# Performance work log

Measured on AMD Instinct MI355X. Metric: run time of the kernel, lower is better.

Reference implementation:

```python
import jax, jax.numpy as jnp
import numpy as np

NTOKENS = 102400
NHID = 128
NTOK_PER_CLASS = 320
NCLASSES = int(np.ceil(NTOKENS / NTOK_PER_CLASS))  # 320
NTOKENS_ACTUAL = NCLASSES * NTOK_PER_CLASS          # 102400
BATCH = 1024


def setup_inputs() -> dict:
    key = jax.random.key(0)
    k1, k2, k3 = jax.random.split(key, 3)
    initrange = 0.1
    return {
        "inputs": jax.random.normal(k1, (BATCH, NHID), dtype=jnp.float32),
        "layer_top_W": jax.random.uniform(k2, (NHID, NCLASSES), dtype=jnp.float32, minval=-initrange, maxval=initrange),
        "layer_top_b": jnp.zeros((NCLASSES,), dtype=jnp.float32),
        "layer_bottom_W": jax.random.uniform(k3, (NTOK_PER_CLASS, NHID), dtype=jnp.float32, minval=-initrange, maxval=initrange),
        "layer_bottom_b": jnp.zeros((NCLASSES,), dtype=jnp.float32),
    }


def reference(inputs, layer_top_W, layer_top_b, layer_bottom_W, layer_bottom_b):
    # labels = arange(ntokens_actual); pos_top = labels // per_class; pos_bottom = labels % per_class
    # The original gathers layer_bottom_W[pos_bottom] ([ntokens_actual, nhid]) before a full matmul;
    # mathematically this is the small matmul inputs @ bottom_W.T tiled nclasses times along dim 1.
    batch = inputs.shape[0]
    pos_bottom_base = jnp.arange(NTOK_PER_CLASS)  # bottom-index pattern within one class block

    layer_top_logits = inputs @ layer_top_W + layer_top_b            # [B, nclasses]
    bottom_block = inputs @ layer_bottom_W.T + layer_bottom_b[pos_bottom_base]  # [B, per_class]

    # repeat_interleave(top, per_class, dim=1) + tile(bottom, nclasses) fused via broadcast:
    target_logits = (layer_top_logits[:, :, None] + bottom_block[:, None, :]).reshape(
        batch, NTOKENS_ACTUAL
    )  # [B, ntokens_actual]
    return target_logits
```

## Files before the change

### kernel.cpp

```cpp
#include <hip/hip_runtime.h>


#define BATCH       1024
#define NHID        128
#define NCLASSES    320
#define PER_CLASS   320
#define ROW_ELEMS   (NCLASSES * PER_CLASS)
#define ROW_F4      (ROW_ELEMS / 4)
#define HALVES      2
#define CLS_PER_BLK (NCLASSES / HALVES)
#define THREADS     320
#define PC_F4       (PER_CLASS / 4)
#define C_PER_ITER  (THREADS / PC_F4)
#define NITER       (CLS_PER_BLK / C_PER_ITER)

typedef float f32x4 __attribute__((ext_vector_type(4)));

__global__ __launch_bounds__(THREADS) void hs_fused_kernel(
    const float* __restrict__ inputs,
    const float* __restrict__ top_W,
    const float* __restrict__ top_b,
    const float* __restrict__ bottom_W,
    const float* __restrict__ bottom_b,
    float* __restrict__ out)
{
    __shared__ __align__(16) float s_in[NHID];
    __shared__ float s_top[CLS_PER_BLK];
    __shared__ __align__(16) float s_bot[PER_CLASS];

    const int b   = blockIdx.x;
    const int h   = blockIdx.y;
    const int tid = threadIdx.x;

    if (tid < NHID) s_in[tid] = inputs[b * NHID + tid];
    __syncthreads();

    for (int j = tid; j < CLS_PER_BLK + PER_CLASS; j += THREADS) {
        float acc;
        if (j < CLS_PER_BLK) {
            const int c = h * CLS_PER_BLK + j;
            acc = top_b[c];
            #pragma unroll 8
            for (int k = 0; k < NHID; ++k)
                acc += s_in[k] * top_W[k * NCLASSES + c];
            s_top[j] = acc;
        } else {
            const int t = j - CLS_PER_BLK;
            acc = bottom_b[t];
            const f32x4* w4 = (const f32x4*)(bottom_W + t * NHID);
            #pragma unroll 8
            for (int k4 = 0; k4 < NHID / 4; ++k4) {
                f32x4 w = w4[k4];
                acc += s_in[4 * k4 + 0] * w.x + s_in[4 * k4 + 1] * w.y
                     + s_in[4 * k4 + 2] * w.z + s_in[4 * k4 + 3] * w.w;
            }
            s_bot[t] = acc;
        }
    }
    __syncthreads();

    const int c_off = tid / PC_F4;
    const int t4    = tid - c_off * PC_F4;
    const f32x4 bv  = ((const f32x4*)s_bot)[t4];

    f32x4* outp = (f32x4*)out
                + (size_t)b * ROW_F4
                + h * (CLS_PER_BLK * PC_F4)
                + c_off * PC_F4 + t4;

    #pragma unroll 8
    for (int it = 0; it < NITER; ++it) {
        const float tv = s_top[it * C_PER_ITER + c_off];
        f32x4 v;
        v.x = tv + bv.x;
        v.y = tv + bv.y;
        v.z = tv + bv.z;
        v.w = tv + bv.w;
        outp[it * (C_PER_ITER * PC_F4)] = v;
    }
}

extern "C" void kernel_launch(void* const* d_in, const int* in_sizes, int n_in,
                              void* d_out, int out_size, void* d_ws, size_t ws_size,
                              hipStream_t stream) {
    const float* inputs   = (const float*)d_in[0];
    const float* top_W    = (const float*)d_in[1];
    const float* top_b    = (const float*)d_in[2];
    const float* bottom_W = (const float*)d_in[3];
    const float* bottom_b = (const float*)d_in[4];
    float* out = (float*)d_out;

    hs_fused_kernel<<<dim3(BATCH, HALVES), THREADS, 0, stream>>>(
        inputs, top_W, top_b, bottom_W, bottom_b, out);
}
```

Baseline: 441.7 us.

## Split into logits kernel plus grid-stride broadcast store kernel via workspace

Splits the work in two. A first kernel computes the top and bottom logits for each batch row into a workspace buffer. A second kernel, run on a fixed grid of 2048 blocks, grid-strides over the output and writes the broadcast sums, so the 400 MB output write is decoupled from the per-row matvec. The old fused kernel is kept as a fallback for when no workspace is available. The cost is an extra launch, integer divisions per element in the store kernel, and small reads of the workspace.

New measurement: 458.2 us. 3.7% more time.

```diff
diff --git a/kernel.cpp b/kernel.cpp
--- a/kernel.cpp
+++ b/kernel.cpp
@@ -1,48 +1,109 @@
 #include <hip/hip_runtime.h>
 
 
-#define BATCH       1024
-#define NHID        128
-#define NCLASSES    320
-#define PER_CLASS   320
-#define ROW_ELEMS   (NCLASSES * PER_CLASS)
-#define ROW_F4      (ROW_ELEMS / 4)
-#define HALVES      2
-#define CLS_PER_BLK (NCLASSES / HALVES)
-#define THREADS     320
-#define PC_F4       (PER_CLASS / 4)
-#define C_PER_ITER  (THREADS / PC_F4)
-#define NITER       (CLS_PER_BLK / C_PER_ITER)
+#define BATCH      1024
+#define NHID       128
+#define NCLASSES   320
+#define PER_CLASS  320
+#define ROW_ELEMS  (NCLASSES * PER_CLASS)
+#define ROW_F4     (ROW_ELEMS / 4)
+#define PC_F4      (PER_CLASS / 4)
+#define LPR        (NCLASSES + PER_CLASS)
+#define LPR_F4     (LPR / 4)
+#define WS_BYTES   ((size_t)BATCH * LPR * sizeof(float))
+
+#define STHREADS   256
+#define SGRID      2048
+#define TOTAL_F4   (BATCH * ROW_F4)
+#define SSTRIDE    (SGRID * STHREADS)
+#define SITERS     (TOTAL_F4 / SSTRIDE)
 
 typedef float f32x4 __attribute__((ext_vector_type(4)));
 
-__global__ __launch_bounds__(THREADS) void hs_fused_kernel(
+__global__ __launch_bounds__(LPR) void hs_logits_kernel(
     const float* __restrict__ inputs,
     const float* __restrict__ top_W,
     const float* __restrict__ top_b,
     const float* __restrict__ bottom_W,
     const float* __restrict__ bottom_b,
-    float* __restrict__ out)
+    float* __restrict__ ws)
 {
     __shared__ __align__(16) float s_in[NHID];
-    __shared__ float s_top[CLS_PER_BLK];
-    __shared__ __align__(16) float s_bot[PER_CLASS];
-
     const int b   = blockIdx.x;
-    const int h   = blockIdx.y;
     const int tid = threadIdx.x;
 
     if (tid < NHID) s_in[tid] = inputs[b * NHID + tid];
     __syncthreads();
 
-    for (int j = tid; j < CLS_PER_BLK + PER_CLASS; j += THREADS) {
+    float acc;
+    if (tid < NCLASSES) {
+        acc = top_b[tid];
+        #pragma unroll 8
+        for (int k = 0; k < NHID; ++k)
+            acc += s_in[k] * top_W[k * NCLASSES + tid];
+    } else {
+        const int t = tid - NCLASSES;
+        acc = bottom_b[t];
+        const f32x4* w4 = (const f32x4*)(bottom_W + t * NHID);
+        #pragma unroll 8
+        for (int k4 = 0; k4 < NHID / 4; ++k4) {
+            f32x4 w = w4[k4];
+            acc += s_in[4*k4+0]*w.x + s_in[4*k4+1]*w.y
+                 + s_in[4*k4+2]*w.z + s_in[4*k4+3]*w.w;
+        }
+    }
+    ws[b * LPR + tid] = acc;
+}
+
+__global__ __launch_bounds__(STHREADS, 8) void hs_stream_kernel(
+    const float* __restrict__ ws,
+    float* __restrict__ out)
+{
+    const f32x4* __restrict__ ws4  = (const f32x4*)ws;
+    f32x4* __restrict__ out4 = (f32x4*)out;
+
+    unsigned g = blockIdx.x * STHREADS + threadIdx.x;
+    #pragma unroll 5
+    for (int it = 0; it < SITERS; ++it, g += SSTRIDE) {
+        const unsigned b  = g / ROW_F4;
+        const unsigned r  = g - b * ROW_F4;
+        const unsigned c  = r / PC_F4;
+        const unsigned t4 = r - c * PC_F4;
+        const float tv = ws[b * LPR + c];
+        const f32x4 bv = ws4[b * LPR_F4 + (NCLASSES/4) + t4];
+        f32x4 v;
+        v.x = tv + bv.x;
+        v.y = tv + bv.y;
+        v.z = tv + bv.z;
+        v.w = tv + bv.w;
+        out4[g] = v;
+    }
+}
+
+#define HALVES      2
+#define CLS_PER_BLK (NCLASSES / HALVES)
+#define FTHREADS    320
+#define C_PER_ITER  (FTHREADS / PC_F4)
+#define NITER       (CLS_PER_BLK / C_PER_ITER)
+
+__global__ __launch_bounds__(FTHREADS) void hs_fused_kernel(
+    const float* __restrict__ inputs, const float* __restrict__ top_W,
+    const float* __restrict__ top_b, const float* __restrict__ bottom_W,
+    const float* __restrict__ bottom_b, float* __restrict__ out)
+{
+    __shared__ __align__(16) float s_in[NHID];
+    __shared__ float s_top[CLS_PER_BLK];
+    __shared__ __align__(16) float s_bot[PER_CLASS];
+    const int b = blockIdx.x, h = blockIdx.y, tid = threadIdx.x;
+    if (tid < NHID) s_in[tid] = inputs[b * NHID + tid];
+    __syncthreads();
+    for (int j = tid; j < CLS_PER_BLK + PER_CLASS; j += FTHREADS) {
         float acc;
         if (j < CLS_PER_BLK) {
             const int c = h * CLS_PER_BLK + j;
             acc = top_b[c];
             #pragma unroll 8
-            for (int k = 0; k < NHID; ++k)
-                acc += s_in[k] * top_W[k * NCLASSES + c];
+            for (int k = 0; k < NHID; ++k) acc += s_in[k] * top_W[k * NCLASSES + c];
             s_top[j] = acc;
         } else {
             const int t = j - CLS_PER_BLK;
@@ -51,31 +112,21 @@
             #pragma unroll 8
             for (int k4 = 0; k4 < NHID / 4; ++k4) {
                 f32x4 w = w4[k4];
-                acc += s_in[4 * k4 + 0] * w.x + s_in[4 * k4 + 1] * w.y
-                     + s_in[4 * k4 + 2] * w.z + s_in[4 * k4 + 3] * w.w;
+                acc += s_in[4*k4+0]*w.x + s_in[4*k4+1]*w.y + s_in[4*k4+2]*w.z + s_in[4*k4+3]*w.w;
             }
             s_bot[t] = acc;
         }
     }
     __syncthreads();
-
     const int c_off = tid / PC_F4;
     const int t4    = tid - c_off * PC_F4;
     const f32x4 bv  = ((const f32x4*)s_bot)[t4];
-
-    f32x4* outp = (f32x4*)out
-                + (size_t)b * ROW_F4
-                + h * (CLS_PER_BLK * PC_F4)
-                + c_off * PC_F4 + t4;
-
+    f32x4* outp = (f32x4*)out + (size_t)b * ROW_F4 + h * (CLS_PER_BLK * PC_F4) + c_off * PC_F4 + t4;
     #pragma unroll 8
     for (int it = 0; it < NITER; ++it) {
         const float tv = s_top[it * C_PER_ITER + c_off];
         f32x4 v;
-        v.x = tv + bv.x;
-        v.y = tv + bv.y;
-        v.z = tv + bv.z;
-        v.w = tv + bv.w;
+        v.x = tv + bv.x; v.y = tv + bv.y; v.z = tv + bv.z; v.w = tv + bv.w;
         outp[it * (C_PER_ITER * PC_F4)] = v;
     }
 }
@@ -90,6 +141,12 @@
     const float* bottom_b = (const float*)d_in[4];
     float* out = (float*)d_out;
 
-    hs_fused_kernel<<<dim3(BATCH, HALVES), THREADS, 0, stream>>>(
-        inputs, top_W, top_b, bottom_W, bottom_b, out);
+    if (d_ws != nullptr && ws_size >= WS_BYTES) {
+        float* ws = (float*)d_ws;
+        hs_logits_kernel<<<BATCH, LPR, 0, stream>>>(inputs, top_W, top_b, bottom_W, bottom_b, ws);
+        hs_stream_kernel<<<SGRID, STHREADS, 0, stream>>>(ws, out);
+    } else {
+        hs_fused_kernel<<<dim3(BATCH, HALVES), FTHREADS, 0, stream>>>(
+            inputs, top_W, top_b, bottom_W, bottom_b, out);
+    }
 }
```
